# Performance work log

Hardware: AMD Instinct MI355X
Metric: run time of the kernel (lower is better)

Reference implementation:

```python
import jax, jax.numpy as jnp
import numpy as np

N_NODES = 100000


def _segment_softmax(logits, seg, num_segments):
    # numerically stable softmax of per-edge logits grouped by destination node
    m = jax.ops.segment_max(logits, seg, num_segments=num_segments)
    e = jnp.exp(logits - m[seg])
    s = jax.ops.segment_sum(e, seg, num_segments=num_segments)
    return e / s[seg]


def _cgat(x, W, b, src, dst, edge_attr, num_nodes):
    # get_edge_att: softmax of edge_attr over edges sharing a destination node
    att = _segment_softmax(edge_attr, dst, num_nodes)
    xw = x @ W.T                                  # [N, out]
    msg = att[:, None] * xw[src]                  # gather + scale  [E, out]
    aggr = jax.ops.segment_sum(msg, dst, num_segments=num_nodes)  # scatter-add
    out = aggr + xw + b                           # update(aggr, x) then + bias
    return jax.nn.sigmoid(out)


def setup_inputs() -> dict:
    key = jax.random.key(0)
    k1, k2, k3, k4, k5, k6 = jax.random.split(key, 6)
    in_c, hid_c, out_c = 128, 64, 64
    n_edges = 1600000
    x = jax.random.normal(k1, (N_NODES, in_c), dtype=jnp.float32)
    edge_index = jax.random.randint(k2, (2, n_edges), 0, N_NODES, dtype=jnp.int64)
    edge_attr = jax.random.uniform(k3, (n_edges,), dtype=jnp.float32)
    W1 = jax.random.normal(k4, (hid_c, in_c), dtype=jnp.float32) / np.sqrt(in_c)
    b1 = jnp.zeros((hid_c,), dtype=jnp.float32)
    W2 = jax.random.normal(k5, (out_c, hid_c), dtype=jnp.float32) / np.sqrt(hid_c)
    b2 = jnp.zeros((out_c,), dtype=jnp.float32)
    return {"x": x, "edge_index": edge_index, "edge_attr": edge_attr,
            "W1": W1, "b1": b1, "W2": W2, "b2": b2}


def reference(x, edge_index, edge_attr, W1, b1, W2, b2):
    src, dst = edge_index[0], edge_index[1]
    h1 = _cgat(x, W1, b1, src, dst, edge_attr, N_NODES)
    h2 = _cgat(h1, W2, b2, src, dst, edge_attr, N_NODES)
    return h2
```

## Files before the change

### kernel.cpp

```cpp
#include <hip/hip_runtime.h>
#include <hip/hip_bf16.h>

#define N_NODES 100000
#define N_EDGES 1600000
#define IN_C 128
#define C 64
#define NBKT 196
#define CAP 9216
#define BCHK 6400
#define NBB (N_EDGES / BCHK)

typedef float vfloat2 __attribute__((ext_vector_type(2)));

__device__ __forceinline__ float bfu2f(unsigned short u) {
    return __uint_as_float(((unsigned int)u) << 16);
}
__device__ __forceinline__ unsigned short f2bfu(float f) {
    __hip_bfloat16 h = __float2bfloat16(f);
    unsigned short u; __builtin_memcpy(&u, &h, 2); return u;
}
__device__ __forceinline__ float blo(unsigned int v) { return __uint_as_float(v << 16); }
__device__ __forceinline__ float bhi(unsigned int v) { return __uint_as_float(v & 0xFFFF0000u); }
__device__ __forceinline__ float dec_w(unsigned int p) {
    return __uint_as_float(((p & 0x7FFFu) + 0x1FC000u) << 9);
}
__device__ __forceinline__ float load_f(const void* p, int i, int f32) {
    return f32 ? ((const float*)p)[i] : bfu2f(((const unsigned short*)p)[i]);
}
__device__ __forceinline__ int load_idx(const void* ei, size_t i, int i64) {
    return i64 ? (int)((const long long*)ei)[i] : ((const int*)ei)[i];
}

__global__ __launch_bounds__(256) void k_detect(
    const uint4* __restrict__ x4, const int* __restrict__ ei32,
    int* __restrict__ flags)
{
    __shared__ int cff, cnz;
    int t = threadIdx.x;
    if (t == 0) { cff = 0; cnz = 0; }
    __syncthreads();
    int lff = 0;
    #pragma unroll
    for (int j = 0; j < 16; ++j) {
        uint4 w = x4[t + j * 256];
        unsigned int a[4] = {w.x, w.y, w.z, w.w};
        #pragma unroll
        for (int q = 0; q < 4; ++q) {
            if ((a[q] & 0x00007F80u) == 0x00007F80u) lff++;
            if ((a[q] & 0x7F800000u) == 0x7F800000u) lff++;
        }
    }
    int lnz = 0;
    for (int i = t; i < 2048; i += 256)
        if (ei32[2 * i + 1] != 0) lnz++;
    if (lff) atomicAdd(&cff, lff);
    if (lnz) atomicAdd(&cnz, lnz);
    __syncthreads();
    if (t == 0) {
        flags[0] = (cff > 0) ? 1 : 0;
        flags[1] = (cnz == 0) ? 1 : 0;
    }
}

__global__ __launch_bounds__(256) void k_bucket(
    const void* __restrict__ ea, const void* __restrict__ ei,
    const int* __restrict__ flags, int* __restrict__ gcnt,
    int2* __restrict__ bkt)
{
    __shared__ int h[NBKT], lrk[NBKT], gbase[NBKT];
    int t = threadIdx.x;
    if (t < NBKT) { h[t] = 0; lrk[t] = 0; }
    __syncthreads();
    int i64 = flags[1], f32 = flags[0];
    int base = blockIdx.x * BCHK;
    for (int i = 0; i < 25; ++i) {
        int e = base + i * 256 + t;
        int d = load_idx(ei, (size_t)N_EDGES + e, i64);
        atomicAdd(&h[d >> 9], 1);
    }
    __syncthreads();
    if (t < NBKT) gbase[t] = atomicAdd(&gcnt[t], h[t]);
    __syncthreads();
    for (int i = 0; i < 25; ++i) {
        int e = base + i * 256 + t;
        int d = load_idx(ei, (size_t)N_EDGES + e, i64);
        int s = load_idx(ei, (size_t)e, i64);
        float w = expf(load_f(ea, e, f32));
        unsigned int wb = __float_as_uint(w);
        int wq = (int)((wb + 0x100u) >> 9) - 0x1FC000;
        wq = wq < 0 ? 0 : (wq > 0x7FFF ? 0x7FFF : wq);
        int b = d >> 9;
        int lr = atomicAdd(&lrk[b], 1);
        int idx = gbase[b] + lr;
        idx = idx < CAP ? idx : CAP - 1;
        bkt[(size_t)b * CAP + idx] =
            make_int2((int)(((unsigned int)s << 15) | (unsigned int)wq), d);
    }
}

__global__ __launch_bounds__(256) void k_bktscan(
    const int* __restrict__ gcnt, int* __restrict__ colbase,
    int* __restrict__ row_ptr)
{
    __shared__ int ps[256];
    int t = threadIdx.x;
    int v = (t < NBKT) ? gcnt[t] : 0;
    ps[t] = v;
    for (int off = 1; off < 256; off <<= 1) {
        __syncthreads();
        int val = (t >= off) ? ps[t - off] : 0;
        __syncthreads();
        ps[t] += val;
    }
    __syncthreads();
    if (t < NBKT) colbase[t] = ps[t] - v;
    if (t == NBKT - 1) colbase[NBKT] = ps[t];
    if (t == 0) row_ptr[N_NODES] = N_EDGES;
}

__global__ __launch_bounds__(256) void k_fine(
    const int2* __restrict__ bkt, const int* __restrict__ gcnt,
    const int* __restrict__ colbase, int* __restrict__ row_ptr,
    unsigned int* __restrict__ srt)
{
    __shared__ int h[512], ex[512], ps[256];
    int t = threadIdx.x, b = blockIdx.x;
    h[t] = 0; h[t + 256] = 0;
    __syncthreads();
    int nrec = gcnt[b];
    nrec = nrec < CAP ? nrec : CAP;
    int cb = colbase[b];
    const int2* bp = bkt + (size_t)b * CAP;
    for (int i = t; i < nrec; i += 256)
        atomicAdd(&h[bp[i].y & 511], 1);
    __syncthreads();
    int s0 = h[2 * t], s1 = h[2 * t + 1];
    ps[t] = s0 + s1;
    for (int off = 1; off < 256; off <<= 1) {
        __syncthreads();
        int val = (t >= off) ? ps[t - off] : 0;
        __syncthreads();
        ps[t] += val;
    }
    __syncthreads();
    int pe = t ? ps[t - 1] : 0;
    ex[2 * t] = pe; ex[2 * t + 1] = pe + s0;
    __syncthreads();
    int d0 = b * 512 + t;
    if (d0 < N_NODES) row_ptr[d0] = cb + ex[t];
    int d1 = d0 + 256;
    if (d1 < N_NODES) row_ptr[d1] = cb + ex[t + 256];
    h[t] = 0; h[t + 256] = 0;
    __syncthreads();
    for (int i = t; i < nrec; i += 256) {
        int2 r = bp[i];
        int dl = r.y & 511;
        int rk = atomicAdd(&h[dl], 1);
        srt[cb + ex[dl] + rk] = (unsigned int)r.x;
    }
}

#define W1_STRIDE (IN_C + 4)
__global__ __launch_bounds__(256) void k_gemm1(
    const void* __restrict__ x, const void* __restrict__ W,
    const int* __restrict__ flags, unsigned short* __restrict__ xw)
{
    __shared__ float Wls[C * W1_STRIDE];
    __shared__ float xs[32 * IN_C];
    int t = threadIdx.x;
    int f32 = flags[0];
    size_t xbase = (size_t)blockIdx.x * 32 * IN_C;
    if (f32) {
        const float* xp = (const float*)x + xbase;
        #pragma unroll
        for (int j = 0; j < 16; ++j) { int i = t + j * 256; xs[i] = xp[i]; }
        const float* wp = (const float*)W;
        #pragma unroll
        for (int j = 0; j < 32; ++j) {
            int i = t + j * 256;
            Wls[(i >> 7) * W1_STRIDE + (i & 127)] = wp[i];
        }
    } else {
        const unsigned int* xp = (const unsigned int*)((const unsigned short*)x + xbase);
        #pragma unroll
        for (int j = 0; j < 8; ++j) {
            int i = t + j * 256;
            unsigned int v = xp[i];
            xs[2 * i]     = blo(v);
            xs[2 * i + 1] = bhi(v);
        }
        const unsigned short* wp = (const unsigned short*)W;
        #pragma unroll
        for (int j = 0; j < 32; ++j) {
            int i = t + j * 256;
            Wls[(i >> 7) * W1_STRIDE + (i & 127)] = bfu2f(wp[i]);
        }
    }
    __syncthreads();
    int col = t & 63, wv = t >> 6;
    const float* wr = Wls + col * W1_STRIDE;
    const float* xr = xs + wv * 8 * IN_C;
    float acc[8];
    #pragma unroll
    for (int n = 0; n < 8; ++n) acc[n] = 0.f;
    #pragma unroll
    for (int kk = 0; kk < IN_C / 4; ++kk) {
        float4 w4 = *(const float4*)(wr + kk * 4);
        #pragma unroll
        for (int n = 0; n < 8; ++n) {
            float4 x4 = *(const float4*)(xr + n * IN_C + kk * 4);
            acc[n] += x4.x * w4.x + x4.y * w4.y + x4.z * w4.z + x4.w * w4.w;
        }
    }
    size_t obase = (size_t)blockIdx.x * 32 * C + wv * 8 * C + col;
    #pragma unroll
    for (int n = 0; n < 8; ++n) xw[obase + n * C] = f2bfu(acc[n]);
}

#define W2_STRIDE (C + 4)
__global__ __launch_bounds__(256) void k_gemm2(
    const unsigned int* __restrict__ h, const void* __restrict__ W,
    const int* __restrict__ flags, unsigned short* __restrict__ xw)
{
    __shared__ float Wls[C * W2_STRIDE];
    __shared__ float xs[32 * C];
    int t = threadIdx.x;
    size_t dwbase = (size_t)blockIdx.x * 32 * 32;
    #pragma unroll
    for (int j = 0; j < 4; ++j) {
        int i = t + j * 256;
        unsigned int v = h[dwbase + i];
        xs[2 * i]     = blo(v);
        xs[2 * i + 1] = bhi(v);
    }
    if (flags[0]) {
        const float* wp = (const float*)W;
        #pragma unroll
        for (int j = 0; j < 16; ++j) {
            int i = t + j * 256;
            Wls[(i >> 6) * W2_STRIDE + (i & 63)] = wp[i];
        }
    } else {
        const unsigned short* wp = (const unsigned short*)W;
        #pragma unroll
        for (int j = 0; j < 16; ++j) {
            int i = t + j * 256;
            Wls[(i >> 6) * W2_STRIDE + (i & 63)] = bfu2f(wp[i]);
        }
    }
    __syncthreads();
    int col = t & 63, wv = t >> 6;
    const float* wr = Wls + col * W2_STRIDE;
    const float* xr = xs + wv * 8 * C;
    float acc[8];
    #pragma unroll
    for (int n = 0; n < 8; ++n) acc[n] = 0.f;
    #pragma unroll
    for (int kk = 0; kk < C / 4; ++kk) {
        float4 w4 = *(const float4*)(wr + kk * 4);
        #pragma unroll
        for (int n = 0; n < 8; ++n) {
            float4 x4 = *(const float4*)(xr + n * C + kk * 4);
            acc[n] += x4.x * w4.x + x4.y * w4.y + x4.z * w4.z + x4.w * w4.w;
        }
    }
    size_t obase = (size_t)blockIdx.x * 32 * C + wv * 8 * C + col;
    #pragma unroll
    for (int n = 0; n < 8; ++n) xw[obase + n * C] = f2bfu(acc[n]);
}

__global__ __launch_bounds__(256) void k_msg_csr(
    const unsigned int* __restrict__ xw, const unsigned int* __restrict__ srt,
    const int* __restrict__ row_ptr, const void* __restrict__ b,
    const int* __restrict__ flags, void* __restrict__ outp, int out_is_final)
{
    int d = blockIdx.x * 4 + (threadIdx.x >> 6);
    int lane = threadIdx.x & 63;
    int half = lane >> 5, li = lane & 31;
    int beg = row_ptr[d], end = row_ptr[d + 1];
    float accx = 0.f, accy = 0.f, asum = 0.f;
    int j = beg;
    for (; j + 8 <= end; j += 8) {
        int jb = j + 4 * half;
        unsigned int p0 = __builtin_nontemporal_load(srt + jb);
        unsigned int p1 = __builtin_nontemporal_load(srt + jb + 1);
        unsigned int p2 = __builtin_nontemporal_load(srt + jb + 2);
        unsigned int p3 = __builtin_nontemporal_load(srt + jb + 3);
        unsigned int v0 = xw[(size_t)(p0 >> 15) * 32 + li];
        unsigned int v1 = xw[(size_t)(p1 >> 15) * 32 + li];
        unsigned int v2 = xw[(size_t)(p2 >> 15) * 32 + li];
        unsigned int v3 = xw[(size_t)(p3 >> 15) * 32 + li];
        float w0 = dec_w(p0), w1 = dec_w(p1), w2 = dec_w(p2), w3 = dec_w(p3);
        accx += w0 * blo(v0) + w1 * blo(v1) + w2 * blo(v2) + w3 * blo(v3);
        accy += w0 * bhi(v0) + w1 * bhi(v1) + w2 * bhi(v2) + w3 * bhi(v3);
        asum += (w0 + w1) + (w2 + w3);
    }
    if (j + 4 <= end) {
        int jb = j + 2 * half;
        unsigned int p0 = __builtin_nontemporal_load(srt + jb);
        unsigned int p1 = __builtin_nontemporal_load(srt + jb + 1);
        unsigned int v0 = xw[(size_t)(p0 >> 15) * 32 + li];
        unsigned int v1 = xw[(size_t)(p1 >> 15) * 32 + li];
        float w0 = dec_w(p0), w1 = dec_w(p1);
        accx += w0 * blo(v0) + w1 * blo(v1);
        accy += w0 * bhi(v0) + w1 * bhi(v1);
        asum += w0 + w1;
        j += 4;
    }
    if (j + 2 <= end) {
        unsigned int p0 = __builtin_nontemporal_load(srt + j + half);
        unsigned int v0 = xw[(size_t)(p0 >> 15) * 32 + li];
        float w0 = dec_w(p0);
        accx += w0 * blo(v0);
        accy += w0 * bhi(v0);
        asum += w0;
        j += 2;
    }
    if (j < end && half == 0) {
        unsigned int p0 = __builtin_nontemporal_load(srt + j);
        unsigned int v0 = xw[(size_t)(p0 >> 15) * 32 + li];
        float w0 = dec_w(p0);
        accx += w0 * blo(v0);
        accy += w0 * bhi(v0);
        asum += w0;
    }
    accx += __shfl_xor(accx, 32);
    accy += __shfl_xor(accy, 32);
    asum += __shfl_xor(asum, 32);
    float inv = (end > beg) ? 1.f / asum : 0.f;
    unsigned int sv = xw[(size_t)d * 32 + li];
    int f32 = flags[0];
    float b0 = load_f(b, 2 * li, f32), b1 = load_f(b, 2 * li + 1, f32);
    float v0 = accx * inv + blo(sv) + b0;
    float v1 = accy * inv + bhi(sv) + b1;
    float r0 = 1.f / (1.f + expf(-v0));
    float r1 = 1.f / (1.f + expf(-v1));
    if (half == 0) {
        if (out_is_final && f32) {
            vfloat2 rv; rv.x = r0; rv.y = r1;
            __builtin_nontemporal_store(rv, (vfloat2*)outp + (size_t)d * 32 + li);
        } else {
            unsigned int packed = (unsigned int)f2bfu(r0) | ((unsigned int)f2bfu(r1) << 16);
            __builtin_nontemporal_store(packed, (unsigned int*)outp + (size_t)d * 32 + li);
        }
    }
}

extern "C" void kernel_launch(void* const* d_in, const int* in_sizes, int n_in,
                              void* d_out, int out_size, void* d_ws, size_t ws_size,
                              hipStream_t stream) {
    const void* x  = d_in[0];
    const void* ei = d_in[1];
    const void* ea = d_in[2];
    const void* W1 = d_in[3];
    const void* b1 = d_in[4];
    const void* W2 = d_in[5];
    const void* b2 = d_in[6];

    char* base = (char*)d_ws;
    int*            flags   = (int*)base;
    int*            gcnt    = (int*)(base + 256);
    int*            colbase = (int*)(base + 1536);
    int*            row_ptr = (int*)(base + 4096);
    unsigned int*   srt     = (unsigned int*)(base + 405504);
    int2*           bkt     = (int2*)(base + 6805504);
    unsigned short* xw      = (unsigned short*)(base + 6805504);
    unsigned short* h1      = (unsigned short*)(base + 19605504);

    k_detect<<<1, 256, 0, stream>>>((const uint4*)x, (const int*)ei, flags);
    hipMemsetAsync(gcnt, 0, 1024, stream);

    k_bucket<<<NBB, 256, 0, stream>>>(ea, ei, flags, gcnt, bkt);
    k_bktscan<<<1, 256, 0, stream>>>(gcnt, colbase, row_ptr);
    k_fine<<<NBKT, 256, 0, stream>>>(bkt, gcnt, colbase, row_ptr, srt);

    k_gemm1<<<N_NODES / 32, 256, 0, stream>>>(x, W1, flags, xw);
    k_msg_csr<<<N_NODES / 4, 256, 0, stream>>>((const unsigned int*)xw, srt, row_ptr, b1, flags, h1, 0);

    k_gemm2<<<N_NODES / 32, 256, 0, stream>>>((const unsigned int*)h1, W2, flags, xw);
    k_msg_csr<<<N_NODES / 4, 256, 0, stream>>>((const unsigned int*)xw, srt, row_ptr, b2, flags, d_out, 1);
}
```

Before: 340.3 us.

## Fuse bucketing with first GEMM and fold bucket scan into fine sort

Merges the edge-bucketing kernel and the first node GEMM into one launch with disjoint block ranges so the two independent stages run concurrently. Bucketing now stages records in shared memory sorted by bucket before writing, which makes the global scatter writes more contiguous. The separate single-block scan kernel is removed, and each fine-sort block recomputes the bucket prefix itself. Workspace is relaid out so xw no longer aliases the bucket buffer. The cost is a large shared-memory footprint for the fused kernel, which may lower occupancy, and redundant scan work in every fine block.

```diff
diff --git a/kernel.cpp b/kernel.cpp
--- a/kernel.cpp
+++ b/kernel.cpp
@@ -9,6 +9,7 @@
 #define CAP 9216
 #define BCHK 6400
 #define NBB (N_EDGES / BCHK)
+#define GB1 (N_NODES / 32)
 
 typedef float vfloat2 __attribute__((ext_vector_type(2)));
 
@@ -62,48 +63,129 @@
     }
 }
 
-__global__ __launch_bounds__(256) void k_bucket(
+#define W1_STRIDE (IN_C + 4)
+__global__ __launch_bounds__(256) void k_build_gemm1(
     const void* __restrict__ ea, const void* __restrict__ ei,
     const int* __restrict__ flags, int* __restrict__ gcnt,
-    int2* __restrict__ bkt)
-{
-    __shared__ int h[NBKT], lrk[NBKT], gbase[NBKT];
+    int2* __restrict__ bkt,
+    const void* __restrict__ x, const void* __restrict__ W,
+    unsigned short* __restrict__ xw)
+{
+    __shared__ __align__(16) char smem[56576];
     int t = threadIdx.x;
-    if (t < NBKT) { h[t] = 0; lrk[t] = 0; }
-    __syncthreads();
-    int i64 = flags[1], f32 = flags[0];
-    int base = blockIdx.x * BCHK;
-    for (int i = 0; i < 25; ++i) {
-        int e = base + i * 256 + t;
-        int d = load_idx(ei, (size_t)N_EDGES + e, i64);
-        atomicAdd(&h[d >> 9], 1);
-    }
-    __syncthreads();
-    if (t < NBKT) gbase[t] = atomicAdd(&gcnt[t], h[t]);
-    __syncthreads();
-    for (int i = 0; i < 25; ++i) {
-        int e = base + i * 256 + t;
-        int d = load_idx(ei, (size_t)N_EDGES + e, i64);
-        int s = load_idx(ei, (size_t)e, i64);
-        float w = expf(load_f(ea, e, f32));
-        unsigned int wb = __float_as_uint(w);
-        int wq = (int)((wb + 0x100u) >> 9) - 0x1FC000;
-        wq = wq < 0 ? 0 : (wq > 0x7FFF ? 0x7FFF : wq);
-        int b = d >> 9;
-        int lr = atomicAdd(&lrk[b], 1);
-        int idx = gbase[b] + lr;
-        idx = idx < CAP ? idx : CAP - 1;
-        bkt[(size_t)b * CAP + idx] =
-            make_int2((int)(((unsigned int)s << 15) | (unsigned int)wq), d);
-    }
-}
-
-__global__ __launch_bounds__(256) void k_bktscan(
-    const int* __restrict__ gcnt, int* __restrict__ colbase,
-    int* __restrict__ row_ptr)
-{
-    __shared__ int ps[256];
-    int t = threadIdx.x;
+    if (blockIdx.x < NBB) {
+        int2* stage = (int2*)smem;
+        int*  h     = (int*)(smem + 51200);
+        int*  ex    = (int*)(smem + 52224);
+        int*  gb    = (int*)(smem + 53248);
+        int*  ps    = (int*)(smem + 54272);
+        int*  rk    = (int*)(smem + 55296);
+        h[t] = 0; rk[t] = 0;
+        __syncthreads();
+        int i64 = flags[1], f32 = flags[0];
+        int base = blockIdx.x * BCHK;
+        for (int i = 0; i < 25; ++i) {
+            int e = base + i * 256 + t;
+            int d = load_idx(ei, (size_t)N_EDGES + e, i64);
+            atomicAdd(&h[d >> 9], 1);
+        }
+        __syncthreads();
+        int hv = h[t];
+        ps[t] = hv;
+        for (int off = 1; off < 256; off <<= 1) {
+            __syncthreads();
+            int val = (t >= off) ? ps[t - off] : 0;
+            __syncthreads();
+            ps[t] += val;
+        }
+        __syncthreads();
+        ex[t] = ps[t] - hv;
+        if (t < NBKT) gb[t] = atomicAdd(&gcnt[t], hv);
+        __syncthreads();
+        for (int i = 0; i < 25; ++i) {
+            int e = base + i * 256 + t;
+            int d = load_idx(ei, (size_t)N_EDGES + e, i64);
+            int s = load_idx(ei, (size_t)e, i64);
+            float w = expf(load_f(ea, e, f32));
+            unsigned int wb = __float_as_uint(w);
+            int wq = (int)((wb + 0x100u) >> 9) - 0x1FC000;
+            wq = wq < 0 ? 0 : (wq > 0x7FFF ? 0x7FFF : wq);
+            int bk2 = d >> 9;
+            int r = atomicAdd(&rk[bk2], 1);
+            stage[ex[bk2] + r] =
+                make_int2((int)(((unsigned int)s << 15) | (unsigned int)wq), d);
+        }
+        __syncthreads();
+        for (int i = 0; i < 25; ++i) {
+            int idx = i * 256 + t;
+            int2 r = stage[idx];
+            int bk2 = ((unsigned int)r.y) >> 9;
+            int lr = idx - ex[bk2];
+            int gi = gb[bk2] + lr;
+            if (gi < CAP)
+                bkt[(size_t)bk2 * CAP + gi] = r;
+        }
+    } else {
+        int bx = blockIdx.x - NBB;
+        float* Wls = (float*)smem;
+        float* xs  = (float*)(smem + 33792);
+        int f32 = flags[0];
+        size_t xbase = (size_t)bx * 32 * IN_C;
+        if (f32) {
+            const float* xp = (const float*)x + xbase;
+            #pragma unroll
+            for (int j = 0; j < 16; ++j) { int i = t + j * 256; xs[i] = xp[i]; }
+            const float* wp = (const float*)W;
+            #pragma unroll
+            for (int j = 0; j < 32; ++j) {
+                int i = t + j * 256;
+                Wls[(i >> 7) * W1_STRIDE + (i & 127)] = wp[i];
+            }
+        } else {
+            const unsigned int* xp = (const unsigned int*)((const unsigned short*)x + xbase);
+            #pragma unroll
+            for (int j = 0; j < 8; ++j) {
+                int i = t + j * 256;
+                unsigned int v = xp[i];
+                xs[2 * i]     = blo(v);
+                xs[2 * i + 1] = bhi(v);
+            }
+            const unsigned short* wp = (const unsigned short*)W;
+            #pragma unroll
+            for (int j = 0; j < 32; ++j) {
+                int i = t + j * 256;
+                Wls[(i >> 7) * W1_STRIDE + (i & 127)] = bfu2f(wp[i]);
+            }
+        }
+        __syncthreads();
+        int col = t & 63, wv = t >> 6;
+        const float* wr = Wls + col * W1_STRIDE;
+        const float* xr = xs + wv * 8 * IN_C;
+        float acc[8];
+        #pragma unroll
+        for (int n = 0; n < 8; ++n) acc[n] = 0.f;
+        #pragma unroll
+        for (int kk = 0; kk < IN_C / 4; ++kk) {
+            float4 w4 = *(const float4*)(wr + kk * 4);
+            #pragma unroll
+            for (int n = 0; n < 8; ++n) {
+                float4 x4 = *(const float4*)(xr + n * IN_C + kk * 4);
+                acc[n] += x4.x * w4.x + x4.y * w4.y + x4.z * w4.z + x4.w * w4.w;
+            }
+        }
+        size_t obase = (size_t)bx * 32 * C + wv * 8 * C + col;
+        #pragma unroll
+        for (int n = 0; n < 8; ++n) xw[obase + n * C] = f2bfu(acc[n]);
+    }
+}
+
+__global__ __launch_bounds__(256) void k_fine(
+    const int2* __restrict__ bkt, const int* __restrict__ gcnt,
+    int* __restrict__ row_ptr, unsigned int* __restrict__ srt)
+{
+    __shared__ int h[512], ex[512], ps[256];
+    __shared__ int sh_cb;
+    int t = threadIdx.x, b = blockIdx.x;
     int v = (t < NBKT) ? gcnt[t] : 0;
     ps[t] = v;
     for (int off = 1; off < 256; off <<= 1) {
@@ -113,23 +195,13 @@
         ps[t] += val;
     }
     __syncthreads();
-    if (t < NBKT) colbase[t] = ps[t] - v;
-    if (t == NBKT - 1) colbase[NBKT] = ps[t];
-    if (t == 0) row_ptr[N_NODES] = N_EDGES;
-}
-
-__global__ __launch_bounds__(256) void k_fine(
-    const int2* __restrict__ bkt, const int* __restrict__ gcnt,
-    const int* __restrict__ colbase, int* __restrict__ row_ptr,
-    unsigned int* __restrict__ srt)
-{
-    __shared__ int h[512], ex[512], ps[256];
-    int t = threadIdx.x, b = blockIdx.x;
+    if (t == b) sh_cb = ps[t] - v;
+    if (b == 0 && t == 0) row_ptr[N_NODES] = N_EDGES;
     h[t] = 0; h[t + 256] = 0;
     __syncthreads();
     int nrec = gcnt[b];
     nrec = nrec < CAP ? nrec : CAP;
-    int cb = colbase[b];
+    int cb = sh_cb;
     const int2* bp = bkt + (size_t)b * CAP;
     for (int i = t; i < nrec; i += 256)
         atomicAdd(&h[bp[i].y & 511], 1);
@@ -158,63 +230,6 @@
         int rk = atomicAdd(&h[dl], 1);
         srt[cb + ex[dl] + rk] = (unsigned int)r.x;
     }
-}
-
-#define W1_STRIDE (IN_C + 4)
-__global__ __launch_bounds__(256) void k_gemm1(
-    const void* __restrict__ x, const void* __restrict__ W,
-    const int* __restrict__ flags, unsigned short* __restrict__ xw)
-{
-    __shared__ float Wls[C * W1_STRIDE];
-    __shared__ float xs[32 * IN_C];
-    int t = threadIdx.x;
-    int f32 = flags[0];
-    size_t xbase = (size_t)blockIdx.x * 32 * IN_C;
-    if (f32) {
-        const float* xp = (const float*)x + xbase;
-        #pragma unroll
-        for (int j = 0; j < 16; ++j) { int i = t + j * 256; xs[i] = xp[i]; }
-        const float* wp = (const float*)W;
-        #pragma unroll
-        for (int j = 0; j < 32; ++j) {
-            int i = t + j * 256;
-            Wls[(i >> 7) * W1_STRIDE + (i & 127)] = wp[i];
-        }
-    } else {
-        const unsigned int* xp = (const unsigned int*)((const unsigned short*)x + xbase);
-        #pragma unroll
-        for (int j = 0; j < 8; ++j) {
-            int i = t + j * 256;
-            unsigned int v = xp[i];
-            xs[2 * i]     = blo(v);
-            xs[2 * i + 1] = bhi(v);
-        }
-        const unsigned short* wp = (const unsigned short*)W;
-        #pragma unroll
-        for (int j = 0; j < 32; ++j) {
-            int i = t + j * 256;
-            Wls[(i >> 7) * W1_STRIDE + (i & 127)] = bfu2f(wp[i]);
-        }
-    }
-    __syncthreads();
-    int col = t & 63, wv = t >> 6;
-    const float* wr = Wls + col * W1_STRIDE;
-    const float* xr = xs + wv * 8 * IN_C;
-    float acc[8];
-    #pragma unroll
-    for (int n = 0; n < 8; ++n) acc[n] = 0.f;
-    #pragma unroll
-    for (int kk = 0; kk < IN_C / 4; ++kk) {
-        float4 w4 = *(const float4*)(wr + kk * 4);
-        #pragma unroll
-        for (int n = 0; n < 8; ++n) {
-            float4 x4 = *(const float4*)(xr + n * IN_C + kk * 4);
-            acc[n] += x4.x * w4.x + x4.y * w4.y + x4.z * w4.z + x4.w * w4.w;
-        }
-    }
-    size_t obase = (size_t)blockIdx.x * 32 * C + wv * 8 * C + col;
-    #pragma unroll
-    for (int n = 0; n < 8; ++n) xw[obase + n * C] = f2bfu(acc[n]);
 }
 
 #define W2_STRIDE (C + 4)
@@ -360,21 +375,19 @@
     char* base = (char*)d_ws;
     int*            flags   = (int*)base;
     int*            gcnt    = (int*)(base + 256);
-    int*            colbase = (int*)(base + 1536);
     int*            row_ptr = (int*)(base + 4096);
     unsigned int*   srt     = (unsigned int*)(base + 405504);
     int2*           bkt     = (int2*)(base + 6805504);
-    unsigned short* xw      = (unsigned short*)(base + 6805504);
-    unsigned short* h1      = (unsigned short*)(base + 19605504);
+    unsigned short* h1      = (unsigned short*)(base + 6805504);
+    unsigned short* xw      = (unsigned short*)(base + 21256192);
 
     k_detect<<<1, 256, 0, stream>>>((const uint4*)x, (const int*)ei, flags);
     hipMemsetAsync(gcnt, 0, 1024, stream);
 
-    k_bucket<<<NBB, 256, 0, stream>>>(ea, ei, flags, gcnt, bkt);
-    k_bktscan<<<1, 256, 0, stream>>>(gcnt, colbase, row_ptr);
-    k_fine<<<NBKT, 256, 0, stream>>>(bkt, gcnt, colbase, row_ptr, srt);
-
-    k_gemm1<<<N_NODES / 32, 256, 0, stream>>>(x, W1, flags, xw);
+    k_build_gemm1<<<NBB + GB1, 256, 0, stream>>>(ea, ei, flags, gcnt, bkt,
+                                                 x, W1, xw);
+    k_fine<<<NBKT, 256, 0, stream>>>(bkt, gcnt, row_ptr, srt);
+
     k_msg_csr<<<N_NODES / 4, 256, 0, stream>>>((const unsigned int*)xw, srt, row_ptr, b1, flags, h1, 0);
 
     k_gemm2<<<N_NODES / 32, 256, 0, stream>>>((const unsigned int*)h1, W2, flags, xw);
```

Result: faster. 324.7 us (-4.6%).
